# Kernel optimization log

Hardware: AMD Instinct MI355X
Metric: run time of the kernel (lower is better)

Reference implementation:

```python
import jax, jax.numpy as jnp
import numpy as np

BLOCK_SIZE = 256


def setup_inputs() -> dict:
    key = jax.random.key(0)
    k1, k2, k3, k4 = jax.random.split(key, 4)
    B, T, C, H = 128, BLOCK_SIZE, 1024, 128
    x = jax.random.normal(k1, (B, T, C), dtype=jnp.float32)
    # nn.Linear(C, H, bias=False): y = x @ W^T with W (H, C); we store W^T as (C, H)
    scale = 1.0 / np.sqrt(C)
    Wq = jax.random.uniform(k2, (C, H), dtype=jnp.float32, minval=-scale, maxval=scale)
    Wk = jax.random.uniform(k3, (C, H), dtype=jnp.float32, minval=-scale, maxval=scale)
    Wv = jax.random.uniform(k4, (C, H), dtype=jnp.float32, minval=-scale, maxval=scale)
    return {"x": x, "Wq": Wq, "Wk": Wk, "Wv": Wv}


def reference(x, Wq, Wk, Wv):
    B, T, C = x.shape
    Q = jnp.einsum('btc,ch->bth', x, Wq)
    K = jnp.einsum('btc,ch->bth', x, Wk)
    V = jnp.einsum('btc,ch->bth', x, Wv)
    d_k = Q.shape[-1]
    scores = jnp.einsum('bth,bsh->bts', Q, K) / jnp.sqrt(jnp.asarray(d_k, x.dtype))
    causal = jnp.tril(jnp.ones((T, T), dtype=bool))  # tril buffer
    scores = jnp.where(causal, scores, -jnp.inf)
    S = jax.nn.softmax(scores, axis=-1)
    out = jnp.einsum('bts,bsh->bth', S, V)
    return out
```

## Files before the change

kernel.cpp:

```cpp
#include <hip/hip_runtime.h>

typedef float  f32x4  __attribute__((ext_vector_type(4)));
typedef short  s16x8  __attribute__((ext_vector_type(8)));
typedef short  s16x4  __attribute__((ext_vector_type(4)));

__device__ __forceinline__ unsigned short f2bf(float f) {
    unsigned int u = __float_as_uint(f);
    return (unsigned short)((u + 0x7FFFu + ((u >> 16) & 1u)) >> 16);
}

__device__ __forceinline__ s16x8 cvt8(f32x4 a, f32x4 b) {
    union { unsigned int u[4]; s16x8 v; } r;
    asm("v_cvt_pk_bf16_f32 %0, %1, %2" : "=v"(r.u[0]) : "v"(a[0]), "v"(a[1]));
    asm("v_cvt_pk_bf16_f32 %0, %1, %2" : "=v"(r.u[1]) : "v"(a[2]), "v"(a[3]));
    asm("v_cvt_pk_bf16_f32 %0, %1, %2" : "=v"(r.u[2]) : "v"(b[0]), "v"(b[1]));
    asm("v_cvt_pk_bf16_f32 %0, %1, %2" : "=v"(r.u[3]) : "v"(b[2]), "v"(b[3]));
    return r.v;
}

#define GLOAD_LDS16(g, l) __builtin_amdgcn_global_load_lds(                    \
    (const __attribute__((address_space(1))) void*)(g),                        \
    (__attribute__((address_space(3))) void*)(l), 16, 0, 0)

__global__ void prep_wt(const float* __restrict__ Wq,
                        const float* __restrict__ Wk,
                        const float* __restrict__ Wv,
                        unsigned char* __restrict__ wt2) {
    int n = blockIdx.x;
    const float* W = (n < 128) ? Wq : ((n < 256) ? Wk : Wv);
    int h = n & 127;
    for (int k = threadIdx.x; k < 1024; k += blockDim.x) {
        unsigned short v = f2bf(W[(size_t)k * 128 + h]);
        size_t off = (size_t)(k >> 6) * 49152 + (size_t)n * 128 +
                     (((k & 63) * 2) ^ ((n & 7) << 4));
        *(unsigned short*)(wt2 + off) = v;
    }
}

__global__ __launch_bounds__(512, 2) void qkv_gemm(
    const float* __restrict__ x,
    const unsigned char* __restrict__ wt2,
    unsigned short* __restrict__ qo,
    unsigned short* __restrict__ ko,
    unsigned short* __restrict__ vto) {

    __shared__ char smem[131072];

    const int tid = threadIdx.x;
    const int bm  = blockIdx.x;
    const int lane = tid & 63, wid = tid >> 6;
    const int lm = lane & 15, l4 = lane >> 4;
    const int wm = wid >> 2, wn = wid & 3;

    f32x4 acc[4][6];
#pragma unroll
    for (int i = 0; i < 4; ++i)
#pragma unroll
        for (int j = 0; j < 6; ++j) acc[i][j] = (f32x4)0.f;

    const int arow = tid >> 2;
    const int acb  = (tid & 3) * 16;
    const float* xp = x + (size_t)(bm * 128 + arow) * 1024 + acb;
    const int aswz = (arow & 7) << 4;
    const int aw0 = arow * 128 + ((acb * 2) ^ aswz);
    const int aw1 = arow * 128 + ((acb * 2 + 16) ^ aswz);

    const int ci0 = wid * 6;
    const unsigned char* wsrc = wt2 + (size_t)ci0 * 1024 + lane * 16;

    int amr[4], bnr[6];
#pragma unroll
    for (int mi = 0; mi < 4; ++mi) amr[mi] = wm * 64 + mi * 16 + lm;
#pragma unroll
    for (int ni = 0; ni < 6; ++ni) bnr[ni] = wn * 96 + ni * 16 + lm;

    {
        f32x4 a0 = *(const f32x4*)(xp);
        f32x4 a1 = *(const f32x4*)(xp + 4);
        f32x4 a2 = *(const f32x4*)(xp + 8);
        f32x4 a3 = *(const f32x4*)(xp + 12);
#pragma unroll
        for (int c = 0; c < 6; ++c)
            GLOAD_LDS16(wsrc + c * 1024, smem + 32768 + (ci0 + c) * 1024);
        *(s16x8*)(smem + aw0) = cvt8(a0, a1);
        *(s16x8*)(smem + aw1) = cvt8(a2, a3);
    }
    __syncthreads();

    for (int ks = 0; ks < 16; ++ks) {
        const int p = ks & 1;
        const int abase = p * 16384;
        const int bbase = 32768 + p * 49152;
        f32x4 n0, n1, n2, n3;
        if (ks < 15) {
            const float* xq = xp + (ks + 1) * 64;
            n0 = *(const f32x4*)(xq);
            n1 = *(const f32x4*)(xq + 4);
            n2 = *(const f32x4*)(xq + 8);
            n3 = *(const f32x4*)(xq + 12);
            const unsigned char* ws = wsrc + (size_t)(ks + 1) * 49152;
#pragma unroll
            for (int c = 0; c < 6; ++c)
                GLOAD_LDS16(ws + c * 1024,
                            smem + 32768 + (p ^ 1) * 49152 + (ci0 + c) * 1024);
        }
#pragma unroll
        for (int kkk = 0; kkk < 2; ++kkk) {
            s16x8 af[4], bf[6];
#pragma unroll
            for (int mi = 0; mi < 4; ++mi)
                af[mi] = *(const s16x8*)(smem + abase + amr[mi] * 128 +
                           ((kkk * 64 + l4 * 16) ^ ((amr[mi] & 7) << 4)));
#pragma unroll
            for (int ni = 0; ni < 6; ++ni)
                bf[ni] = *(const s16x8*)(smem + bbase + bnr[ni] * 128 +
                           ((kkk * 64 + l4 * 16) ^ ((bnr[ni] & 7) << 4)));
            __builtin_amdgcn_s_setprio(1);
#pragma unroll
            for (int ni = 0; ni < 6; ++ni)
#pragma unroll
                for (int mi = 0; mi < 4; ++mi)
                    acc[mi][ni] = __builtin_amdgcn_mfma_f32_16x16x32_bf16(
                        af[mi], bf[ni], acc[mi][ni], 0, 0, 0);
            __builtin_amdgcn_s_setprio(0);
        }
        if (ks < 15) {
            *(s16x8*)(smem + (abase ^ 16384) + aw0) = cvt8(n0, n1);
            *(s16x8*)(smem + (abase ^ 16384) + aw1) = cvt8(n2, n3);
        }
        __syncthreads();
    }

#pragma unroll
    for (int mi = 0; mi < 4; ++mi) {
        int m0 = bm * 128 + wm * 64 + mi * 16 + l4 * 4;
#pragma unroll
        for (int ni = 0; ni < 6; ++ni) {
            int nb  = wn * 96 + ni * 16;
            int mat = nb >> 7;
            int col = (nb & 127) + lm;
            if (mat == 2) {
                int bb = m0 >> 8, t = m0 & 255;
                s16x4 w4;
#pragma unroll
                for (int j = 0; j < 4; ++j) w4[j] = (short)f2bf(acc[mi][ni][j]);
                *(s16x4*)(vto + ((size_t)bb * 128 + col) * 256 + t) = w4;
            } else {
                unsigned short* dst = (mat == 0) ? qo : ko;
#pragma unroll
                for (int j = 0; j < 4; ++j)
                    dst[(size_t)(m0 + j) * 128 + col] = f2bf(acc[mi][ni][j]);
            }
        }
    }
}

__global__ __launch_bounds__(512) void attn(
    const unsigned short* __restrict__ q,
    const unsigned short* __restrict__ k,
    const unsigned short* __restrict__ vt,
    float* __restrict__ out) {

    __shared__ char pbuf[65536];

    const int tid = threadIdx.x, wid = tid >> 6, lane = tid & 63;
    const int lm = lane & 15, l4 = lane >> 4;
    const int b = blockIdx.x >> 1, qt = blockIdx.x & 1;
    const int qbase = qt << 7;
    const int t0 = qbase + wid * 16;
    const int nfrags = (qbase + 128) >> 4;
    const int nkf    = (qbase + 128) >> 5;

    const unsigned short* qrow = q + (size_t)(b * 256 + t0 + lm) * 128 + l4 * 8;
    s16x8 qf[4];
#pragma unroll
    for (int kf = 0; kf < 4; ++kf) qf[kf] = *(const s16x8*)(qrow + kf * 32);

    f32x4 sacc[16];
#pragma unroll
    for (int i = 0; i < 16; ++i) sacc[i] = (f32x4)0.f;

    const unsigned short* kbase = k + (size_t)(b * 256) * 128 + l4 * 8;
#pragma unroll
    for (int nf = 0; nf < 16; ++nf) {
        if (nf < nfrags) {
#pragma unroll
            for (int kf = 0; kf < 4; ++kf) {
                s16x8 a = *(const s16x8*)(kbase + (size_t)(nf * 16 + lm) * 128 + kf * 32);
                sacc[nf] = __builtin_amdgcn_mfma_f32_16x16x32_bf16(a, qf[kf], sacc[nf], 0, 0, 0);
            }
        }
    }

    const float scale = 0.08838834764831845f;
    const int tg = t0 + lm;
    float mx = -1e30f;
#pragma unroll
    for (int nf = 0; nf < 16; ++nf) {
        if (nf < nfrags) {
#pragma unroll
            for (int j = 0; j < 4; ++j) {
                int kv = nf * 16 + l4 * 4 + j;
                float s = sacc[nf][j] * scale;
                s = (kv > tg) ? -1e30f : s;
                sacc[nf][j] = s;
                mx = fmaxf(mx, s);
            }
        }
    }
    mx = fmaxf(mx, __shfl_xor(mx, 16));
    mx = fmaxf(mx, __shfl_xor(mx, 32));
    float sum = 0.f;
#pragma unroll
    for (int nf = 0; nf < 16; ++nf) {
        if (nf < nfrags) {
#pragma unroll
            for (int j = 0; j < 4; ++j) {
                float p = __expf(sacc[nf][j] - mx);
                sacc[nf][j] = p;
                sum += p;
            }
        }
    }
    sum += __shfl_xor(sum, 16);
    sum += __shfl_xor(sum, 32);
    float rinv = 1.0f / sum;

    char* pw = pbuf + wid * 8192 + lm * 512;
#pragma unroll
    for (int nf = 0; nf < 16; ++nf) {
        if (nf < nfrags) {
            s16x4 w;
#pragma unroll
            for (int j = 0; j < 4; ++j) w[j] = (short)f2bf(sacc[nf][j] * rinv);
            *(s16x4*)(pw + ((nf * 32 + l4 * 8) ^ ((lm & 7) << 4))) = w;
        }
    }
    asm volatile("s_waitcnt lgkmcnt(0)" ::: "memory");

    f32x4 oacc[8];
#pragma unroll
    for (int i = 0; i < 8; ++i) oacc[i] = (f32x4)0.f;

    const unsigned short* vbase = vt + (size_t)b * 32768 + l4 * 8;
#pragma unroll
    for (int kvf = 0; kvf < 8; ++kvf) {
        if (kvf < nkf) {
            s16x8 pf = *(const s16x8*)(pbuf + wid * 8192 + lm * 512 +
                        ((kvf * 64 + l4 * 16) ^ ((lm & 7) << 4)));
#pragma unroll
            for (int hf = 0; hf < 8; ++hf) {
                s16x8 a = *(const s16x8*)(vbase + (size_t)(hf * 16 + lm) * 256 + kvf * 32);
                oacc[hf] = __builtin_amdgcn_mfma_f32_16x16x32_bf16(a, pf, oacc[hf], 0, 0, 0);
            }
        }
    }

    float* ob = out + (size_t)(b * 256 + t0 + lm) * 128 + l4 * 4;
#pragma unroll
    for (int hf = 0; hf < 8; ++hf)
        *(f32x4*)(ob + hf * 16) = oacc[hf];
}

extern "C" void kernel_launch(void* const* d_in, const int* in_sizes, int n_in,
                              void* d_out, int out_size, void* d_ws, size_t ws_size,
                              hipStream_t stream) {
    const float* x  = (const float*)d_in[0];
    const float* Wq = (const float*)d_in[1];
    const float* Wk = (const float*)d_in[2];
    const float* Wv = (const float*)d_in[3];
    float* out = (float*)d_out;

    char* ws = (char*)d_ws;
    unsigned char*  wt = (unsigned char*)(ws);
    unsigned short* qb = (unsigned short*)(ws + 786432);
    unsigned short* kb = (unsigned short*)(ws + 786432 + 8388608);
    unsigned short* vb = (unsigned short*)(ws + 786432 + 2 * 8388608);

    prep_wt<<<384, 256, 0, stream>>>(Wq, Wk, Wv, wt);
    qkv_gemm<<<256, 512, 0, stream>>>(x, wt, qb, kb, vb);
    attn<<<256, 512, 0, stream>>>(qb, kb, vb, out);
}
```

Measured before the change: 78.69 us.

## Retile QKV GEMM warps to 128x48 and replace syncthreads with finer waitcnt pipeline

Each warp now covers all 128 rows and a 48-column slice instead of a 64x96 sub-tile, so every warp loads its own contiguous block of W rows. The k-step is split into two halves, and the next W tile's direct-to-LDS loads are issued between them. Full __syncthreads are replaced with explicit s_waitcnt vmcnt/lgkmcnt plus s_barrier, so only the needed loads are waited on. This aims to overlap global loads with MFMA work and cut barrier stalls. The cost is more A-fragment LDS reads per warp (8 A vs 3 B), and hand-counted vmcnt values are fragile.

Measured after the change: 82.98 us. 5.5% more time.

```diff
diff --git a/kernel.cpp b/kernel.cpp
--- a/kernel.cpp
+++ b/kernel.cpp
@@ -50,13 +50,12 @@
     const int bm  = blockIdx.x;
     const int lane = tid & 63, wid = tid >> 6;
     const int lm = lane & 15, l4 = lane >> 4;
-    const int wm = wid >> 2, wn = wid & 3;
-
-    f32x4 acc[4][6];
-#pragma unroll
-    for (int i = 0; i < 4; ++i)
-#pragma unroll
-        for (int j = 0; j < 6; ++j) acc[i][j] = (f32x4)0.f;
+
+    f32x4 acc[8][3];
+#pragma unroll
+    for (int i = 0; i < 8; ++i)
+#pragma unroll
+        for (int j = 0; j < 3; ++j) acc[i][j] = (f32x4)0.f;
 
     const int arow = tid >> 2;
     const int acb  = (tid & 3) * 16;
@@ -65,86 +64,113 @@
     const int aw0 = arow * 128 + ((acb * 2) ^ aswz);
     const int aw1 = arow * 128 + ((acb * 2 + 16) ^ aswz);
 
-    const int ci0 = wid * 6;
-    const unsigned char* wsrc = wt2 + (size_t)ci0 * 1024 + lane * 16;
-
-    int amr[4], bnr[6];
-#pragma unroll
-    for (int mi = 0; mi < 4; ++mi) amr[mi] = wm * 64 + mi * 16 + lm;
-#pragma unroll
-    for (int ni = 0; ni < 6; ++ni) bnr[ni] = wn * 96 + ni * 16 + lm;
+    const unsigned char* wsrc = wt2 +
+        (size_t)(wid * 48 + (lane >> 3)) * 128 + (lane & 7) * 16;
+    const int bldsrow = (wid * 48) * 128;
+
+    int amr[8], bnr[3];
+#pragma unroll
+    for (int mi = 0; mi < 8; ++mi) amr[mi] = mi * 16 + lm;
+#pragma unroll
+    for (int ni = 0; ni < 3; ++ni) bnr[ni] = wid * 48 + ni * 16 + lm;
 
     {
-        f32x4 a0 = *(const f32x4*)(xp);
-        f32x4 a1 = *(const f32x4*)(xp + 4);
-        f32x4 a2 = *(const f32x4*)(xp + 8);
-        f32x4 a3 = *(const f32x4*)(xp + 12);
+        f32x4 q0 = *(const f32x4*)(xp);
+        f32x4 q1 = *(const f32x4*)(xp + 4);
+        f32x4 q2 = *(const f32x4*)(xp + 8);
+        f32x4 q3 = *(const f32x4*)(xp + 12);
 #pragma unroll
         for (int c = 0; c < 6; ++c)
-            GLOAD_LDS16(wsrc + c * 1024, smem + 32768 + (ci0 + c) * 1024);
-        *(s16x8*)(smem + aw0) = cvt8(a0, a1);
-        *(s16x8*)(smem + aw1) = cvt8(a2, a3);
-    }
-    __syncthreads();
-
-    for (int ks = 0; ks < 16; ++ks) {
-        const int p = ks & 1;
-        const int abase = p * 16384;
-        const int bbase = 32768 + p * 49152;
+            GLOAD_LDS16(wsrc + c * 1024, smem + 32768 + bldsrow + c * 1024);
+        asm volatile("s_waitcnt vmcnt(6)" ::: "memory");
+        *(s16x8*)(smem + aw0) = cvt8(q0, q1);
+        *(s16x8*)(smem + aw1) = cvt8(q2, q3);
+        asm volatile("s_waitcnt lgkmcnt(0)" ::: "memory");
+        __builtin_amdgcn_s_barrier();
+    }
+
+    for (int t = 0; t < 16; ++t) {
+        const int ab = (t & 1) * 16384;
+        const int bb = 32768 + (t & 1) * 49152;
         f32x4 n0, n1, n2, n3;
-        if (ks < 15) {
-            const float* xq = xp + (ks + 1) * 64;
+        if (t < 15) {
+            const float* xq = xp + (t + 1) * 64;
             n0 = *(const f32x4*)(xq);
             n1 = *(const f32x4*)(xq + 4);
             n2 = *(const f32x4*)(xq + 8);
             n3 = *(const f32x4*)(xq + 12);
-            const unsigned char* ws = wsrc + (size_t)(ks + 1) * 49152;
-#pragma unroll
-            for (int c = 0; c < 6; ++c)
-                GLOAD_LDS16(ws + c * 1024,
-                            smem + 32768 + (p ^ 1) * 49152 + (ci0 + c) * 1024);
-        }
-#pragma unroll
-        for (int kkk = 0; kkk < 2; ++kkk) {
-            s16x8 af[4], bf[6];
-#pragma unroll
-            for (int mi = 0; mi < 4; ++mi)
-                af[mi] = *(const s16x8*)(smem + abase + amr[mi] * 128 +
-                           ((kkk * 64 + l4 * 16) ^ ((amr[mi] & 7) << 4)));
-#pragma unroll
-            for (int ni = 0; ni < 6; ++ni)
-                bf[ni] = *(const s16x8*)(smem + bbase + bnr[ni] * 128 +
-                           ((kkk * 64 + l4 * 16) ^ ((bnr[ni] & 7) << 4)));
+            asm volatile("s_waitcnt vmcnt(4)" ::: "memory");
+        } else {
+            asm volatile("s_waitcnt vmcnt(0)" ::: "memory");
+        }
+        {
+            s16x8 af[8], bf[3];
+#pragma unroll
+            for (int mi = 0; mi < 8; ++mi)
+                af[mi] = *(const s16x8*)(smem + ab + amr[mi] * 128 +
+                           ((l4 * 16) ^ ((amr[mi] & 7) << 4)));
+#pragma unroll
+            for (int ni = 0; ni < 3; ++ni)
+                bf[ni] = *(const s16x8*)(smem + bb + bnr[ni] * 128 +
+                           ((l4 * 16) ^ ((bnr[ni] & 7) << 4)));
             __builtin_amdgcn_s_setprio(1);
 #pragma unroll
-            for (int ni = 0; ni < 6; ++ni)
-#pragma unroll
-                for (int mi = 0; mi < 4; ++mi)
+            for (int ni = 0; ni < 3; ++ni)
+#pragma unroll
+                for (int mi = 0; mi < 8; ++mi)
                     acc[mi][ni] = __builtin_amdgcn_mfma_f32_16x16x32_bf16(
                         af[mi], bf[ni], acc[mi][ni], 0, 0, 0);
             __builtin_amdgcn_s_setprio(0);
         }
-        if (ks < 15) {
-            *(s16x8*)(smem + (abase ^ 16384) + aw0) = cvt8(n0, n1);
-            *(s16x8*)(smem + (abase ^ 16384) + aw1) = cvt8(n2, n3);
-        }
-        __syncthreads();
-    }
-
-#pragma unroll
-    for (int mi = 0; mi < 4; ++mi) {
-        int m0 = bm * 128 + wm * 64 + mi * 16 + l4 * 4;
-#pragma unroll
-        for (int ni = 0; ni < 6; ++ni) {
-            int nb  = wn * 96 + ni * 16;
+        if (t < 15) {
+            const unsigned char* ws = wsrc + (size_t)(t + 1) * 49152;
+            char* bdst = smem + 32768 + ((t & 1) ^ 1) * 49152 + bldsrow;
+#pragma unroll
+            for (int c = 0; c < 6; ++c)
+                GLOAD_LDS16(ws + c * 1024, bdst + c * 1024);
+        }
+        {
+            s16x8 af[8], bf[3];
+#pragma unroll
+            for (int mi = 0; mi < 8; ++mi)
+                af[mi] = *(const s16x8*)(smem + ab + amr[mi] * 128 +
+                           ((64 + l4 * 16) ^ ((amr[mi] & 7) << 4)));
+#pragma unroll
+            for (int ni = 0; ni < 3; ++ni)
+                bf[ni] = *(const s16x8*)(smem + bb + bnr[ni] * 128 +
+                           ((64 + l4 * 16) ^ ((bnr[ni] & 7) << 4)));
+            __builtin_amdgcn_s_setprio(1);
+#pragma unroll
+            for (int ni = 0; ni < 3; ++ni)
+#pragma unroll
+                for (int mi = 0; mi < 8; ++mi)
+                    acc[mi][ni] = __builtin_amdgcn_mfma_f32_16x16x32_bf16(
+                        af[mi], bf[ni], acc[mi][ni], 0, 0, 0);
+            __builtin_amdgcn_s_setprio(0);
+        }
+        if (t < 15) {
+            asm volatile("s_waitcnt vmcnt(6)" ::: "memory");
+            *(s16x8*)(smem + (ab ^ 16384) + aw0) = cvt8(n0, n1);
+            *(s16x8*)(smem + (ab ^ 16384) + aw1) = cvt8(n2, n3);
+            asm volatile("s_waitcnt lgkmcnt(0)" ::: "memory");
+            __builtin_amdgcn_s_barrier();
+        }
+    }
+
+#pragma unroll
+    for (int mi = 0; mi < 8; ++mi) {
+        int m0 = bm * 128 + mi * 16 + l4 * 4;
+#pragma unroll
+        for (int ni = 0; ni < 3; ++ni) {
+            int nb  = wid * 48 + ni * 16;
             int mat = nb >> 7;
             int col = (nb & 127) + lm;
             if (mat == 2) {
-                int bb = m0 >> 8, t = m0 & 255;
+                int bb2 = m0 >> 8, tt = m0 & 255;
                 s16x4 w4;
 #pragma unroll
                 for (int j = 0; j < 4; ++j) w4[j] = (short)f2bf(acc[mi][ni][j]);
-                *(s16x4*)(vto + ((size_t)bb * 128 + col) * 256 + t) = w4;
+                *(s16x4*)(vto + ((size_t)bb2 * 128 + col) * 256 + tt) = w4;
             } else {
                 unsigned short* dst = (mat == 0) ? qo : ko;
 #pragma unroll
```

## Software-pipeline QKV projection GEMM with split phases and explicit barriers

Applied to the files above, without the earlier changes.

Rewrites the QKV projection main loop as a manually unrolled, phase-split schedule. Each k-step is split into two halves, and each half's weight global-to-LDS loads are interleaved with the MFMA cluster. Fine-grained s_barrier and s_waitcnt replace __syncthreads, and x is prefetched into registers one stage further ahead. The aim is to hide global and LDS latency behind matrix work. The cost is much more complex manual synchronisation with hand-tuned vmcnt values, which could be fragile.

Result: slower. 89.56 us (+13.8%).

```diff
diff --git a/kernel.cpp b/kernel.cpp
--- a/kernel.cpp
+++ b/kernel.cpp
@@ -66,70 +66,141 @@
     const int aw1 = arow * 128 + ((acb * 2 + 16) ^ aswz);
 
     const int ci0 = wid * 6;
-    const unsigned char* wsrc = wt2 + (size_t)ci0 * 1024 + lane * 16;
+    const unsigned char* wsrc = wt2 +
+        (size_t)(wid * 48 + (lane >> 3)) * 128 + (lane & 7) * 16;
 
     int amr[4], bnr[6];
 #pragma unroll
     for (int mi = 0; mi < 4; ++mi) amr[mi] = wm * 64 + mi * 16 + lm;
 #pragma unroll
     for (int ni = 0; ni < 6; ++ni) bnr[ni] = wn * 96 + ni * 16 + lm;
+
+    s16x8 af[4], bf[6];
+    f32x4 pA0, pA1, pA2, pA3;
+    f32x4 pB0, pB1, pB2, pB3;
+
+#define PHASE_READS(ABUF, BBUF, KOFF)                                          \
+    do {                                                                       \
+        _Pragma("unroll")                                                      \
+        for (int mi = 0; mi < 4; ++mi)                                         \
+            af[mi] = *(const s16x8*)(smem + (ABUF) + amr[mi] * 128 +           \
+                      (((KOFF) + l4 * 16) ^ ((amr[mi] & 7) << 4)));            \
+        _Pragma("unroll")                                                      \
+        for (int ni = 0; ni < 6; ++ni)                                         \
+            bf[ni] = *(const s16x8*)(smem + (BBUF) + bnr[ni] * 128 +           \
+                      (((KOFF) + l4 * 16) ^ ((bnr[ni] & 7) << 4)));            \
+    } while (0)
+
+#define MFMA_CLUSTER()                                                         \
+    do {                                                                       \
+        __builtin_amdgcn_s_setprio(1);                                         \
+        _Pragma("unroll")                                                      \
+        for (int ni = 0; ni < 6; ++ni)                                         \
+            _Pragma("unroll")                                                  \
+            for (int mi = 0; mi < 4; ++mi)                                     \
+                acc[mi][ni] = __builtin_amdgcn_mfma_f32_16x16x32_bf16(         \
+                    af[mi], bf[ni], acc[mi][ni], 0, 0, 0);                     \
+        __builtin_amdgcn_s_setprio(0);                                         \
+    } while (0)
+
+#define GSTAGE(TNEXT, BDST, C0)                                                \
+    do {                                                                       \
+        const unsigned char* ws_ = wsrc + (size_t)(TNEXT) * 49152;             \
+        _Pragma("unroll")                                                      \
+        for (int c = (C0); c < (C0) + 3; ++c)                                  \
+            GLOAD_LDS16(ws_ + c * 1024, smem + (BDST) + (ci0 + c) * 1024);     \
+    } while (0)
+
+#define BAR() __builtin_amdgcn_s_barrier()
+#define LGKM0() asm volatile("s_waitcnt lgkmcnt(0)" ::: "memory")
 
     {
         f32x4 a0 = *(const f32x4*)(xp);
         f32x4 a1 = *(const f32x4*)(xp + 4);
         f32x4 a2 = *(const f32x4*)(xp + 8);
         f32x4 a3 = *(const f32x4*)(xp + 12);
-#pragma unroll
-        for (int c = 0; c < 6; ++c)
-            GLOAD_LDS16(wsrc + c * 1024, smem + 32768 + (ci0 + c) * 1024);
+        GSTAGE(0, 32768, 0);
+        GSTAGE(0, 32768, 3);
+        pA0 = *(const f32x4*)(xp + 64);
+        pA1 = *(const f32x4*)(xp + 68);
+        pA2 = *(const f32x4*)(xp + 72);
+        pA3 = *(const f32x4*)(xp + 76);
         *(s16x8*)(smem + aw0) = cvt8(a0, a1);
         *(s16x8*)(smem + aw1) = cvt8(a2, a3);
-    }
-    __syncthreads();
-
-    for (int ks = 0; ks < 16; ++ks) {
-        const int p = ks & 1;
-        const int abase = p * 16384;
-        const int bbase = 32768 + p * 49152;
-        f32x4 n0, n1, n2, n3;
-        if (ks < 15) {
-            const float* xq = xp + (ks + 1) * 64;
-            n0 = *(const f32x4*)(xq);
-            n1 = *(const f32x4*)(xq + 4);
-            n2 = *(const f32x4*)(xq + 8);
-            n3 = *(const f32x4*)(xq + 12);
-            const unsigned char* ws = wsrc + (size_t)(ks + 1) * 49152;
-#pragma unroll
-            for (int c = 0; c < 6; ++c)
-                GLOAD_LDS16(ws + c * 1024,
-                            smem + 32768 + (p ^ 1) * 49152 + (ci0 + c) * 1024);
-        }
-#pragma unroll
-        for (int kkk = 0; kkk < 2; ++kkk) {
-            s16x8 af[4], bf[6];
-#pragma unroll
-            for (int mi = 0; mi < 4; ++mi)
-                af[mi] = *(const s16x8*)(smem + abase + amr[mi] * 128 +
-                           ((kkk * 64 + l4 * 16) ^ ((amr[mi] & 7) << 4)));
-#pragma unroll
-            for (int ni = 0; ni < 6; ++ni)
-                bf[ni] = *(const s16x8*)(smem + bbase + bnr[ni] * 128 +
-                           ((kkk * 64 + l4 * 16) ^ ((bnr[ni] & 7) << 4)));
-            __builtin_amdgcn_s_setprio(1);
-#pragma unroll
-            for (int ni = 0; ni < 6; ++ni)
-#pragma unroll
-                for (int mi = 0; mi < 4; ++mi)
-                    acc[mi][ni] = __builtin_amdgcn_mfma_f32_16x16x32_bf16(
-                        af[mi], bf[ni], acc[mi][ni], 0, 0, 0);
-            __builtin_amdgcn_s_setprio(0);
-        }
-        if (ks < 15) {
-            *(s16x8*)(smem + (abase ^ 16384) + aw0) = cvt8(n0, n1);
-            *(s16x8*)(smem + (abase ^ 16384) + aw1) = cvt8(n2, n3);
-        }
-        __syncthreads();
-    }
+        asm volatile("s_waitcnt vmcnt(4)" ::: "memory");
+        LGKM0();
+        BAR();
+    }
+
+    for (int ti = 0; ti < 7; ++ti) {
+        const int t = 2 * ti;
+        PHASE_READS(0, 32768, 0);
+        GSTAGE(t + 1, 81920, 0);
+        BAR(); LGKM0();
+        MFMA_CLUSTER();
+        BAR();
+        PHASE_READS(0, 32768, 64);
+        GSTAGE(t + 1, 81920, 3);
+        {
+            const float* xq = xp + (t + 2) * 64;
+            pB0 = *(const f32x4*)(xq);
+            pB1 = *(const f32x4*)(xq + 4);
+            pB2 = *(const f32x4*)(xq + 8);
+            pB3 = *(const f32x4*)(xq + 12);
+        }
+        *(s16x8*)(smem + 16384 + aw0) = cvt8(pA0, pA1);
+        *(s16x8*)(smem + 16384 + aw1) = cvt8(pA2, pA3);
+        asm volatile("s_waitcnt vmcnt(4) lgkmcnt(0)" ::: "memory");
+        BAR();
+        MFMA_CLUSTER();
+        BAR();
+        PHASE_READS(16384, 81920, 0);
+        GSTAGE(t + 2, 32768, 0);
+        BAR(); LGKM0();
+        MFMA_CLUSTER();
+        BAR();
+        PHASE_READS(16384, 81920, 64);
+        GSTAGE(t + 2, 32768, 3);
+        {
+            const float* xq = xp + (t + 3) * 64;
+            pA0 = *(const f32x4*)(xq);
+            pA1 = *(const f32x4*)(xq + 4);
+            pA2 = *(const f32x4*)(xq + 8);
+            pA3 = *(const f32x4*)(xq + 12);
+        }
+        *(s16x8*)(smem + aw0) = cvt8(pB0, pB1);
+        *(s16x8*)(smem + aw1) = cvt8(pB2, pB3);
+        asm volatile("s_waitcnt vmcnt(4) lgkmcnt(0)" ::: "memory");
+        BAR();
+        MFMA_CLUSTER();
+        BAR();
+    }
+
+    PHASE_READS(0, 32768, 0);
+    GSTAGE(15, 81920, 0);
+    BAR(); LGKM0();
+    MFMA_CLUSTER();
+    BAR();
+    PHASE_READS(0, 32768, 64);
+    GSTAGE(15, 81920, 3);
+    *(s16x8*)(smem + 16384 + aw0) = cvt8(pA0, pA1);
+    *(s16x8*)(smem + 16384 + aw1) = cvt8(pA2, pA3);
+    asm volatile("s_waitcnt vmcnt(0) lgkmcnt(0)" ::: "memory");
+    BAR();
+    MFMA_CLUSTER();
+    BAR();
+    PHASE_READS(16384, 81920, 0);
+    LGKM0();
+    MFMA_CLUSTER();
+    PHASE_READS(16384, 81920, 64);
+    LGKM0();
+    MFMA_CLUSTER();
+
+#undef PHASE_READS
+#undef MFMA_CLUSTER
+#undef GSTAGE
+#undef BAR
+#undef LGKM0
 
 #pragma unroll
     for (int mi = 0; mi < 4; ++mi) {
@@ -140,11 +211,11 @@
             int mat = nb >> 7;
             int col = (nb & 127) + lm;
             if (mat == 2) {
-                int bb = m0 >> 8, t = m0 & 255;
+                int bb2 = m0 >> 8, tt = m0 & 255;
                 s16x4 w4;
 #pragma unroll
                 for (int j = 0; j < 4; ++j) w4[j] = (short)f2bf(acc[mi][ni][j]);
-                *(s16x4*)(vto + ((size_t)bb * 128 + col) * 256 + t) = w4;
+                *(s16x4*)(vto + ((size_t)bb2 * 128 + col) * 256 + tt) = w4;
             } else {
                 unsigned short* dst = (mat == 0) ? qo : ko;
 #pragma unroll
```

## Use 1024-thread QKV GEMM blocks with two-stage-ahead x prefetch and manual waitcnt

Applied to the files above, without the earlier changes.

The QKV projection GEMM now launches 1024 threads (16 waves) per 128-row tile, with each wave covering 48 output columns instead of 96, so per-thread accumulators are halved. The fp32 x tile is prefetched two k-steps ahead into registers. The full __syncthreads is replaced with explicit s_waitcnt vmcnt/lgkmcnt plus s_barrier so outstanding global loads can overlap the MFMA work. The aim is more waves to hide latency and less stalling at barriers, at the cost of more threads contending at each barrier and smaller per-wave MFMA reuse.

New measurement: 79.18 us. About the same (+0.6%).

```diff
diff --git a/kernel.cpp b/kernel.cpp
--- a/kernel.cpp
+++ b/kernel.cpp
@@ -37,7 +37,7 @@
     }
 }
 
-__global__ __launch_bounds__(512, 2) void qkv_gemm(
+__global__ __launch_bounds__(1024, 4) void qkv_gemm(
     const float* __restrict__ x,
     const unsigned char* __restrict__ wt2,
     unsigned short* __restrict__ qo,
@@ -50,101 +50,103 @@
     const int bm  = blockIdx.x;
     const int lane = tid & 63, wid = tid >> 6;
     const int lm = lane & 15, l4 = lane >> 4;
-    const int wm = wid >> 2, wn = wid & 3;
-
-    f32x4 acc[4][6];
+    const int wm = wid >> 3, wn = wid & 7;
+
+    f32x4 acc[4][3];
 #pragma unroll
     for (int i = 0; i < 4; ++i)
 #pragma unroll
-        for (int j = 0; j < 6; ++j) acc[i][j] = (f32x4)0.f;
-
-    const int arow = tid >> 2;
-    const int acb  = (tid & 3) * 16;
-    const float* xp = x + (size_t)(bm * 128 + arow) * 1024 + acb;
-    const int aswz = (arow & 7) << 4;
-    const int aw0 = arow * 128 + ((acb * 2) ^ aswz);
-    const int aw1 = arow * 128 + ((acb * 2 + 16) ^ aswz);
-
-    const int ci0 = wid * 6;
-    const unsigned char* wsrc = wt2 + (size_t)ci0 * 1024 + lane * 16;
-
-    int amr[4], bnr[6];
+        for (int j = 0; j < 3; ++j) acc[i][j] = (f32x4)0.f;
+
+    const int ar  = tid >> 3;
+    const int ac8 = tid & 7;
+    const float* xp = x + (size_t)(bm * 128 + ar) * 1024 + ac8 * 8;
+    const int aw = ar * 128 + ((ac8 * 16) ^ ((ar & 7) << 4));
+
+    const int ci0 = wid * 3;
+    const unsigned char* bsrc = wt2 + (size_t)ci0 * 1024 + (size_t)lane * 16;
+
+    int amr[4], bnr[3];
 #pragma unroll
     for (int mi = 0; mi < 4; ++mi) amr[mi] = wm * 64 + mi * 16 + lm;
 #pragma unroll
-    for (int ni = 0; ni < 6; ++ni) bnr[ni] = wn * 96 + ni * 16 + lm;
+    for (int ni = 0; ni < 3; ++ni) bnr[ni] = wn * 48 + ni * 16 + lm;
+
+    f32x4 pa0, pa1;
 
     {
         f32x4 a0 = *(const f32x4*)(xp);
         f32x4 a1 = *(const f32x4*)(xp + 4);
-        f32x4 a2 = *(const f32x4*)(xp + 8);
-        f32x4 a3 = *(const f32x4*)(xp + 12);
-#pragma unroll
-        for (int c = 0; c < 6; ++c)
-            GLOAD_LDS16(wsrc + c * 1024, smem + 32768 + (ci0 + c) * 1024);
-        *(s16x8*)(smem + aw0) = cvt8(a0, a1);
-        *(s16x8*)(smem + aw1) = cvt8(a2, a3);
-    }
-    __syncthreads();
-
-    for (int ks = 0; ks < 16; ++ks) {
-        const int p = ks & 1;
-        const int abase = p * 16384;
-        const int bbase = 32768 + p * 49152;
-        f32x4 n0, n1, n2, n3;
-        if (ks < 15) {
-            const float* xq = xp + (ks + 1) * 64;
-            n0 = *(const f32x4*)(xq);
-            n1 = *(const f32x4*)(xq + 4);
-            n2 = *(const f32x4*)(xq + 8);
-            n3 = *(const f32x4*)(xq + 12);
-            const unsigned char* ws = wsrc + (size_t)(ks + 1) * 49152;
-#pragma unroll
-            for (int c = 0; c < 6; ++c)
-                GLOAD_LDS16(ws + c * 1024,
-                            smem + 32768 + (p ^ 1) * 49152 + (ci0 + c) * 1024);
+#pragma unroll
+        for (int c = 0; c < 3; ++c)
+            GLOAD_LDS16(bsrc + c * 1024, smem + 32768 + (ci0 + c) * 1024);
+        *(s16x8*)(smem + aw) = cvt8(a0, a1);
+        pa0 = *(const f32x4*)(xp + 64);
+        pa1 = *(const f32x4*)(xp + 68);
+        asm volatile("s_waitcnt vmcnt(2)" ::: "memory");
+        asm volatile("s_waitcnt lgkmcnt(0)" ::: "memory");
+        __builtin_amdgcn_s_barrier();
+    }
+
+    for (int t = 0; t < 16; ++t) {
+        const int p   = t & 1;
+        const int ab  = p * 16384,       bb  = 32768 + p * 49152;
+        const int ab2 = (p ^ 1) * 16384, bb2 = 32768 + (p ^ 1) * 49152;
+        if (t < 15) {
+            const unsigned char* ws = bsrc + (size_t)(t + 1) * 49152;
+#pragma unroll
+            for (int c = 0; c < 3; ++c)
+                GLOAD_LDS16(ws + c * 1024, smem + bb2 + (ci0 + c) * 1024);
         }
 #pragma unroll
         for (int kkk = 0; kkk < 2; ++kkk) {
-            s16x8 af[4], bf[6];
+            s16x8 af[4], bf[3];
 #pragma unroll
             for (int mi = 0; mi < 4; ++mi)
-                af[mi] = *(const s16x8*)(smem + abase + amr[mi] * 128 +
+                af[mi] = *(const s16x8*)(smem + ab + amr[mi] * 128 +
                            ((kkk * 64 + l4 * 16) ^ ((amr[mi] & 7) << 4)));
 #pragma unroll
-            for (int ni = 0; ni < 6; ++ni)
-                bf[ni] = *(const s16x8*)(smem + bbase + bnr[ni] * 128 +
+            for (int ni = 0; ni < 3; ++ni)
+                bf[ni] = *(const s16x8*)(smem + bb + bnr[ni] * 128 +
                            ((kkk * 64 + l4 * 16) ^ ((bnr[ni] & 7) << 4)));
             __builtin_amdgcn_s_setprio(1);
 #pragma unroll
-            for (int ni = 0; ni < 6; ++ni)
+            for (int ni = 0; ni < 3; ++ni)
 #pragma unroll
                 for (int mi = 0; mi < 4; ++mi)
                     acc[mi][ni] = __builtin_amdgcn_mfma_f32_16x16x32_bf16(
                         af[mi], bf[ni], acc[mi][ni], 0, 0, 0);
             __builtin_amdgcn_s_setprio(0);
         }
-        if (ks < 15) {
-            *(s16x8*)(smem + (abase ^ 16384) + aw0) = cvt8(n0, n1);
-            *(s16x8*)(smem + (abase ^ 16384) + aw1) = cvt8(n2, n3);
-        }
-        __syncthreads();
+        if (t < 15) {
+            *(s16x8*)(smem + ab2 + aw) = cvt8(pa0, pa1);
+            if (t < 14) {
+                const float* xq = xp + (t + 2) * 64;
+                pa0 = *(const f32x4*)(xq);
+                pa1 = *(const f32x4*)(xq + 4);
+                asm volatile("s_waitcnt vmcnt(2)" ::: "memory");
+            } else {
+                asm volatile("s_waitcnt vmcnt(0)" ::: "memory");
+            }
+            asm volatile("s_waitcnt lgkmcnt(0)" ::: "memory");
+            __builtin_amdgcn_s_barrier();
+        }
     }
 
 #pragma unroll
     for (int mi = 0; mi < 4; ++mi) {
         int m0 = bm * 128 + wm * 64 + mi * 16 + l4 * 4;
 #pragma unroll
-        for (int ni = 0; ni < 6; ++ni) {
-            int nb  = wn * 96 + ni * 16;
+        for (int ni = 0; ni < 3; ++ni) {
+            int nb  = wn * 48 + ni * 16;
             int mat = nb >> 7;
             int col = (nb & 127) + lm;
             if (mat == 2) {
-                int bb = m0 >> 8, t = m0 & 255;
+                int bb2_ = m0 >> 8, tt = m0 & 255;
                 s16x4 w4;
 #pragma unroll
                 for (int j = 0; j < 4; ++j) w4[j] = (short)f2bf(acc[mi][ni][j]);
-                *(s16x4*)(vto + ((size_t)bb * 128 + col) * 256 + t) = w4;
+                *(s16x4*)(vto + ((size_t)bb2_ * 128 + col) * 256 + tt) = w4;
             } else {
                 unsigned short* dst = (mat == 0) ? qo : ko;
 #pragma unroll
@@ -278,6 +280,6 @@
     unsigned short* vb = (unsigned short*)(ws + 786432 + 2 * 8388608);
 
     prep_wt<<<384, 256, 0, stream>>>(Wq, Wk, Wv, wt);
-    qkv_gemm<<<256, 512, 0, stream>>>(x, wt, qb, kb, vb);
+    qkv_gemm<<<256, 1024, 0, stream>>>(x, wt, qb, kb, vb);
     attn<<<256, 512, 0, stream>>>(qb, kb, vb, out);
 }
```
